# Optimization experiments

Measured on AMD Instinct MI355X. Metric: run time of the kernel, lower is better.

Reference implementation:

```python
import jax, jax.numpy as jnp
import numpy as np


def _filt2d(img, k):
    # 2D cross-correlation with OpenCV's default BORDER_REFLECT_101 padding.
    # img: [H, W], k: [3, 3]. XLA conv is cross-correlation (no flip), matching cv2.
    p = jnp.pad(img, 1, mode='reflect')  # reflect == REFLECT_101
    return jax.lax.conv_general_dilated(p[None, None], k[None, None],
                                        window_strides=(1, 1), padding='VALID')[0, 0]


def setup_inputs() -> dict:
    key = jax.random.key(0)
    k1, k2 = jax.random.split(key)
    pred = jax.random.normal(k1, (1, 1, 4096, 4096), dtype=jnp.float32)
    target = jax.random.normal(k2, (1, 1, 4096, 4096), dtype=jnp.float32)
    return {"pred": pred, "target": target}


def reference(pred, target):
    alpha = 0.2  # forward default
    # ---- masked MSE over target > 0 (named MAE in the original) ----
    valid = target > 0
    diff = jnp.where(valid, target - pred, 0.0)
    n_valid = jnp.maximum(jnp.sum(valid), 1)
    mae = jnp.sum(diff * diff) / n_valid.astype(diff.dtype)
    # ---- edge term: GaussianBlur(3x3, sigma=0) then Sobel x/y (cv2 semantics) ----
    g1 = jnp.array([0.25, 0.5, 0.25], jnp.float32)  # cv2 fixed 3-tap Gaussian
    blur_k = jnp.outer(g1, g1)
    smooth = jnp.array([1.0, 2.0, 1.0], jnp.float32)
    deriv = jnp.array([-1.0, 0.0, 1.0], jnp.float32)
    sob_x = jnp.outer(smooth, deriv)   # d/dx: smooth rows, differentiate cols
    sob_y = jnp.outer(deriv, smooth)   # d/dy
    p2 = jnp.squeeze(pred)   # [H, W]
    t2 = jnp.squeeze(target)
    pb = _filt2d(p2, blur_k)
    tb = _filt2d(t2, blur_k)
    dx = _filt2d(pb, sob_x) - _filt2d(tb, sob_x)
    dy = _filt2d(pb, sob_y) - _filt2d(tb, sob_y)
    # NOTE: original subtracts the y term (as written in the source) — kept faithfully.
    G = jnp.mean(dx * dx - dy * dy)
    # In torch the edge term goes through a numpy round-trip (no gradient).
    G = jax.lax.stop_gradient(G)
    return alpha * G + (1.0 - alpha) * mae
```

## Files before the change

kernel.cpp:

```cpp
#include <hip/hip_runtime.h>


#define TW 256
#define TH 32
#define LROWS 36
#define LW 264

__device__ __forceinline__ int reflect101(int i, int n) {
    if (i < 0) i = -i;
    if (i >= n) i = 2 * n - 2 - i;
    return i;
}

__device__ __forceinline__ void async16(const float* g, float* l) {
    __builtin_amdgcn_global_load_lds(
        (const __attribute__((address_space(1))) void*)g,
        (__attribute__((address_space(3))) void*)l,
        16, 0, 0);
}

__global__ __launch_bounds__(256) void loss_main(
    const float* __restrict__ pred, const float* __restrict__ target,
    double* __restrict__ part, int H, int W)
{
    __shared__ float psh[LROWS][LW];
    __shared__ float tsh[LROWS][LW];
    __shared__ float partials[4][3];

    const int tid  = threadIdx.x;
    const int lane = tid & 63;
    const int w    = tid >> 6;
    const int r0 = blockIdx.y * TH;
    const int c0 = blockIdx.x * TW;

#pragma unroll
    for (int j = 0; j < 18; ++j) {
        const int idx = j * 4 + w;
        const int row = (j >= 9) ? idx - 36 : idx;
        const int gr  = reflect101(r0 - 2 + row, H);
        const size_t goff = (size_t)gr * W + c0 + lane * 4;
        if (j >= 9) async16(target + goff, &tsh[row][4]);
        else        async16(pred   + goff, &psh[row][4]);
    }

    if (tid < 144) {
        const int row = tid >> 2;
        const int hc  = tid & 3;
        const int lc  = (hc < 2) ? (2 + hc) : (258 + hc);
        const int gc  = reflect101((hc < 2) ? (c0 - 2 + hc)
                                            : (c0 + 254 + hc), W);
        const int gr  = reflect101(r0 - 2 + row, H);
        const size_t off = (size_t)gr * W + gc;
        psh[row][lc] = pred[off];
        tsh[row][lc] = target[off];
    }
    __syncthreads();

    const int cg = lane;
    const int rb = w * 8;
    float mse = 0.f, cnt = 0.f, g = 0.f;

    float4 D0, D1, D2, D3, D4, S0, S1, S2, S3, S4;

    auto hpass = [&](int rw, bool doMse, float4& D_, float4& S_) {
        const float4 p0 = *(const float4*)&psh[rw][4 * cg];
        const float4 p1 = *(const float4*)&psh[rw][4 * cg + 4];
        const float4 p2 = *(const float4*)&psh[rw][4 * cg + 8];
        const float4 t0 = *(const float4*)&tsh[rw][4 * cg];
        const float4 t1 = *(const float4*)&tsh[rw][4 * cg + 4];
        const float4 t2 = *(const float4*)&tsh[rw][4 * cg + 8];
        const float e0z = p0.z - t0.z, e0w = p0.w - t0.w;
        const float e1x = p1.x - t1.x, e1y = p1.y - t1.y;
        const float e1z = p1.z - t1.z, e1w = p1.w - t1.w;
        const float e2x = p2.x - t2.x, e2y = p2.y - t2.y;
        D_.x = 0.25f * (e1z - e0z) + 0.5f * (e1y - e0w);
        D_.y = 0.25f * (e1w - e0w) + 0.5f * (e1z - e1x);
        D_.z = 0.25f * (e2x - e1x) + 0.5f * (e1w - e1y);
        D_.w = 0.25f * (e2y - e1y) + 0.5f * (e2x - e1z);
        S_.x = 0.25f * (e0z + e1z) + (e0w + e1y) + 1.5f * e1x;
        S_.y = 0.25f * (e0w + e1w) + (e1x + e1z) + 1.5f * e1y;
        S_.z = 0.25f * (e1x + e2x) + (e1y + e1w) + 1.5f * e1z;
        S_.w = 0.25f * (e1y + e2y) + (e1z + e2x) + 1.5f * e1w;
        if (doMse) {
            if (t1.x > 0.f) { mse += e1x * e1x; cnt += 1.f; }
            if (t1.y > 0.f) { mse += e1y * e1y; cnt += 1.f; }
            if (t1.z > 0.f) { mse += e1z * e1z; cnt += 1.f; }
            if (t1.w > 0.f) { mse += e1w * e1w; cnt += 1.f; }
        }
    };

    hpass(rb + 0, false, D0, S0);
    hpass(rb + 1, false, D1, S1);
    hpass(rb + 2, true,  D2, S2);
    hpass(rb + 3, true,  D3, S3);

#pragma unroll
    for (int k = 0; k < 8; ++k) {
        hpass(rb + 4 + k, (k < 6), D4, S4);
        const float dx0 = 0.25f * (D0.x + D4.x) + (D1.x + D3.x) + 1.5f * D2.x;
        const float dx1 = 0.25f * (D0.y + D4.y) + (D1.y + D3.y) + 1.5f * D2.y;
        const float dx2 = 0.25f * (D0.z + D4.z) + (D1.z + D3.z) + 1.5f * D2.z;
        const float dx3 = 0.25f * (D0.w + D4.w) + (D1.w + D3.w) + 1.5f * D2.w;
        const float dy0 = 0.25f * (S4.x - S0.x) + 0.5f * (S3.x - S1.x);
        const float dy1 = 0.25f * (S4.y - S0.y) + 0.5f * (S3.y - S1.y);
        const float dy2 = 0.25f * (S4.z - S0.z) + 0.5f * (S3.z - S1.z);
        const float dy3 = 0.25f * (S4.w - S0.w) + 0.5f * (S3.w - S1.w);
        g += (dx0 * dx0 - dy0 * dy0) + (dx1 * dx1 - dy1 * dy1)
           + (dx2 * dx2 - dy2 * dy2) + (dx3 * dx3 - dy3 * dy3);
        D0 = D1; D1 = D2; D2 = D3; D3 = D4;
        S0 = S1; S1 = S2; S2 = S3; S3 = S4;
    }

    for (int off = 32; off > 0; off >>= 1) {
        mse += __shfl_down(mse, off, 64);
        cnt += __shfl_down(cnt, off, 64);
        g   += __shfl_down(g,   off, 64);
    }
    if (lane == 0) {
        partials[w][0] = mse;
        partials[w][1] = cnt;
        partials[w][2] = g;
    }
    __syncthreads();
    if (tid == 0) {
        float m = 0.f, c2 = 0.f, gg = 0.f;
        for (int wv = 0; wv < 4; ++wv) {
            m  += partials[wv][0];
            c2 += partials[wv][1];
            gg += partials[wv][2];
        }
        const int bid = blockIdx.y * gridDim.x + blockIdx.x;
        double* slot = part + 3 * bid;
        slot[0] = (double)m;
        slot[1] = (double)c2;
        slot[2] = (double)gg;
    }
}

__global__ __launch_bounds__(256) void loss_final(
    const double* __restrict__ part, int nslots,
    float* __restrict__ out, double inv_hw)
{
    __shared__ double red[4][3];
    double m = 0.0, c = 0.0, g = 0.0;
    for (int s = threadIdx.x; s < nslots; s += 256) {
        m += part[3 * s];
        c += part[3 * s + 1];
        g += part[3 * s + 2];
    }
    for (int off = 32; off > 0; off >>= 1) {
        m += __shfl_down(m, off, 64);
        c += __shfl_down(c, off, 64);
        g += __shfl_down(g, off, 64);
    }
    const int w = threadIdx.x >> 6;
    if ((threadIdx.x & 63) == 0) { red[w][0] = m; red[w][1] = c; red[w][2] = g; }
    __syncthreads();
    if (threadIdx.x == 0) {
        m = red[0][0] + red[1][0] + red[2][0] + red[3][0];
        c = red[0][1] + red[1][1] + red[2][1] + red[3][1];
        g = red[0][2] + red[1][2] + red[2][2] + red[3][2];
        const double cnt = c < 1.0 ? 1.0 : c;
        out[0] = (float)(0.2 * (g * inv_hw) + 0.8 * (m / cnt));
    }
}

extern "C" void kernel_launch(void* const* d_in, const int* in_sizes, int n_in,
                              void* d_out, int out_size, void* d_ws, size_t ws_size,
                              hipStream_t stream) {
    const float* pred   = (const float*)d_in[0];
    const float* target = (const float*)d_in[1];
    float* out   = (float*)d_out;
    double* part = (double*)d_ws;

    const int H = 4096, W = 4096;
    const int nblocks = (W / TW) * (H / TH);

    dim3 grid(W / TW, H / TH);
    loss_main<<<grid, 256, 0, stream>>>(pred, target, part, H, W);
    loss_final<<<1, 256, 0, stream>>>(part, nblocks, out,
                                      1.0 / ((double)H * (double)W));
}
```

Baseline: 147.0 us.

## Stage pred-target difference in single LDS tile via register loads

Replaces the async global-to-LDS loads of separate pred and target tiles with register float4 loads. The difference pred-target is computed once and stored in a single shared tile, relying on linearity of the filters. The masked MSE is computed during the staging pass, halving LDS footprint and LDS reads in the stencil pass. It trades the async direct-to-LDS path for register staging, which raises register pressure (18 float4 held) but may improve occupancy through the smaller LDS use.

```diff
diff --git a/kernel.cpp b/kernel.cpp
--- a/kernel.cpp
+++ b/kernel.cpp
@@ -12,19 +12,11 @@
     return i;
 }
 
-__device__ __forceinline__ void async16(const float* g, float* l) {
-    __builtin_amdgcn_global_load_lds(
-        (const __attribute__((address_space(1))) void*)g,
-        (__attribute__((address_space(3))) void*)l,
-        16, 0, 0);
-}
-
 __global__ __launch_bounds__(256) void loss_main(
     const float* __restrict__ pred, const float* __restrict__ target,
     double* __restrict__ part, int H, int W)
 {
-    __shared__ float psh[LROWS][LW];
-    __shared__ float tsh[LROWS][LW];
+    __shared__ float esh[LROWS][LW];
     __shared__ float partials[4][3];
 
     const int tid  = threadIdx.x;
@@ -33,70 +25,79 @@
     const int r0 = blockIdx.y * TH;
     const int c0 = blockIdx.x * TW;
 
-#pragma unroll
-    for (int j = 0; j < 18; ++j) {
-        const int idx = j * 4 + w;
-        const int row = (j >= 9) ? idx - 36 : idx;
-        const int gr  = reflect101(r0 - 2 + row, H);
-        const size_t goff = (size_t)gr * W + c0 + lane * 4;
-        if (j >= 9) async16(target + goff, &tsh[row][4]);
-        else        async16(pred   + goff, &psh[row][4]);
+    float mse = 0.f, cnt = 0.f, g = 0.f;
+
+    float hp = 0.f, ht = 0.f;
+    int hrow = 0, hlc = 0;
+    const bool hasHalo = (tid < 144);
+    if (hasHalo) {
+        hrow = tid >> 2;
+        const int hc = tid & 3;
+        hlc = (hc < 2) ? (2 + hc) : (258 + hc);
+        const int gc = reflect101((hc < 2) ? (c0 - 2 + hc)
+                                           : (c0 + 254 + hc), W);
+        const int gr = reflect101(r0 - 2 + hrow, H);
+        const size_t off = (size_t)gr * W + gc;
+        hp = pred[off];
+        ht = target[off];
     }
 
-    if (tid < 144) {
-        const int row = tid >> 2;
-        const int hc  = tid & 3;
-        const int lc  = (hc < 2) ? (2 + hc) : (258 + hc);
-        const int gc  = reflect101((hc < 2) ? (c0 - 2 + hc)
-                                            : (c0 + 254 + hc), W);
+    float4 pv[9], tv[9];
+#pragma unroll
+    for (int j = 0; j < 9; ++j) {
+        const int row = j * 4 + w;
         const int gr  = reflect101(r0 - 2 + row, H);
-        const size_t off = (size_t)gr * W + gc;
-        psh[row][lc] = pred[off];
-        tsh[row][lc] = target[off];
+        const size_t off = (size_t)gr * W + c0 + lane * 4;
+        pv[j] = *(const float4*)(pred   + off);
+        tv[j] = *(const float4*)(target + off);
     }
+#pragma unroll
+    for (int j = 0; j < 9; ++j) {
+        const int row = j * 4 + w;
+        float4 e;
+        e.x = pv[j].x - tv[j].x;
+        e.y = pv[j].y - tv[j].y;
+        e.z = pv[j].z - tv[j].z;
+        e.w = pv[j].w - tv[j].w;
+        *(float4*)&esh[row][4 + 4 * lane] = e;
+        if (row >= 2 && row < 34) {
+            if (tv[j].x > 0.f) { mse += e.x * e.x; cnt += 1.f; }
+            if (tv[j].y > 0.f) { mse += e.y * e.y; cnt += 1.f; }
+            if (tv[j].z > 0.f) { mse += e.z * e.z; cnt += 1.f; }
+            if (tv[j].w > 0.f) { mse += e.w * e.w; cnt += 1.f; }
+        }
+    }
+    if (hasHalo) esh[hrow][hlc] = hp - ht;
+
     __syncthreads();
 
     const int cg = lane;
     const int rb = w * 8;
-    float mse = 0.f, cnt = 0.f, g = 0.f;
 
     float4 D0, D1, D2, D3, D4, S0, S1, S2, S3, S4;
 
-    auto hpass = [&](int rw, bool doMse, float4& D_, float4& S_) {
-        const float4 p0 = *(const float4*)&psh[rw][4 * cg];
-        const float4 p1 = *(const float4*)&psh[rw][4 * cg + 4];
-        const float4 p2 = *(const float4*)&psh[rw][4 * cg + 8];
-        const float4 t0 = *(const float4*)&tsh[rw][4 * cg];
-        const float4 t1 = *(const float4*)&tsh[rw][4 * cg + 4];
-        const float4 t2 = *(const float4*)&tsh[rw][4 * cg + 8];
-        const float e0z = p0.z - t0.z, e0w = p0.w - t0.w;
-        const float e1x = p1.x - t1.x, e1y = p1.y - t1.y;
-        const float e1z = p1.z - t1.z, e1w = p1.w - t1.w;
-        const float e2x = p2.x - t2.x, e2y = p2.y - t2.y;
-        D_.x = 0.25f * (e1z - e0z) + 0.5f * (e1y - e0w);
-        D_.y = 0.25f * (e1w - e0w) + 0.5f * (e1z - e1x);
-        D_.z = 0.25f * (e2x - e1x) + 0.5f * (e1w - e1y);
-        D_.w = 0.25f * (e2y - e1y) + 0.5f * (e2x - e1z);
-        S_.x = 0.25f * (e0z + e1z) + (e0w + e1y) + 1.5f * e1x;
-        S_.y = 0.25f * (e0w + e1w) + (e1x + e1z) + 1.5f * e1y;
-        S_.z = 0.25f * (e1x + e2x) + (e1y + e1w) + 1.5f * e1z;
-        S_.w = 0.25f * (e1y + e2y) + (e1z + e2x) + 1.5f * e1w;
-        if (doMse) {
-            if (t1.x > 0.f) { mse += e1x * e1x; cnt += 1.f; }
-            if (t1.y > 0.f) { mse += e1y * e1y; cnt += 1.f; }
-            if (t1.z > 0.f) { mse += e1z * e1z; cnt += 1.f; }
-            if (t1.w > 0.f) { mse += e1w * e1w; cnt += 1.f; }
-        }
+    auto hpass = [&](int rw, float4& D_, float4& S_) {
+        const float4 a = *(const float4*)&esh[rw][4 * cg];
+        const float4 b = *(const float4*)&esh[rw][4 * cg + 4];
+        const float4 c = *(const float4*)&esh[rw][4 * cg + 8];
+        D_.x = 0.25f * (b.z - a.z) + 0.5f * (b.y - a.w);
+        D_.y = 0.25f * (b.w - a.w) + 0.5f * (b.z - b.x);
+        D_.z = 0.25f * (c.x - b.x) + 0.5f * (b.w - b.y);
+        D_.w = 0.25f * (c.y - b.y) + 0.5f * (c.x - b.z);
+        S_.x = 0.25f * (a.z + b.z) + (a.w + b.y) + 1.5f * b.x;
+        S_.y = 0.25f * (a.w + b.w) + (b.x + b.z) + 1.5f * b.y;
+        S_.z = 0.25f * (b.x + c.x) + (b.y + b.w) + 1.5f * b.z;
+        S_.w = 0.25f * (b.y + c.y) + (b.z + c.x) + 1.5f * b.w;
     };
 
-    hpass(rb + 0, false, D0, S0);
-    hpass(rb + 1, false, D1, S1);
-    hpass(rb + 2, true,  D2, S2);
-    hpass(rb + 3, true,  D3, S3);
+    hpass(rb + 0, D0, S0);
+    hpass(rb + 1, D1, S1);
+    hpass(rb + 2, D2, S2);
+    hpass(rb + 3, D3, S3);
 
 #pragma unroll
     for (int k = 0; k < 8; ++k) {
-        hpass(rb + 4 + k, (k < 6), D4, S4);
+        hpass(rb + 4 + k, D4, S4);
         const float dx0 = 0.25f * (D0.x + D4.x) + (D1.x + D3.x) + 1.5f * D2.x;
         const float dx1 = 0.25f * (D0.y + D4.y) + (D1.y + D3.y) + 1.5f * D2.y;
         const float dx2 = 0.25f * (D0.z + D4.z) + (D1.z + D3.z) + 1.5f * D2.z;
```

After: 150.0 us. 1.02x slower.

## Make blocks persistent over tile columns with double-buffered async LDS loads

Applied to the files above, without the earlier changes.

Each block now has 512 threads and walks 8 vertically stacked 256x32 tiles. It double-buffers the pred/target LDS tiles, issuing async global-to-LDS loads for tile i+2 while tile i is computed, and uses explicit vmcnt/lgkmcnt waits and s_barrier. This is meant to hide global load latency behind compute and to reduce per-block launch and halo overhead. The costs are far fewer blocks (256), one block per CU because of the doubled LDS, and fragile hand-written wait counts.

```diff
diff --git a/kernel.cpp b/kernel.cpp
--- a/kernel.cpp
+++ b/kernel.cpp
@@ -5,6 +5,7 @@
 #define TH 32
 #define LROWS 36
 #define LW 264
+#define NT 8
 
 __device__ __forceinline__ int reflect101(int i, int n) {
     if (i < 0) i = -i;
@@ -15,100 +16,137 @@
 __device__ __forceinline__ void async16(const float* g, float* l) {
     __builtin_amdgcn_global_load_lds(
         (const __attribute__((address_space(1))) void*)g,
-        (__attribute__((address_space(3))) void*)l,
-        16, 0, 0);
-}
-
-__global__ __launch_bounds__(256) void loss_main(
+        (__attribute__((address_space(3))) void*)l, 16, 0, 0);
+}
+
+#define SFENCE()  __builtin_amdgcn_sched_barrier(0)
+#define BAR()     asm volatile("s_barrier" ::: "memory")
+#define VMCNT10() asm volatile("s_waitcnt vmcnt(10)" ::: "memory")
+#define VMCNT0()  asm volatile("s_waitcnt vmcnt(0)" ::: "memory")
+#define LGKM0()   asm volatile("s_waitcnt lgkmcnt(0)" ::: "memory")
+
+__global__ __launch_bounds__(512, 1) void loss_main(
     const float* __restrict__ pred, const float* __restrict__ target,
     double* __restrict__ part, int H, int W)
 {
-    __shared__ float psh[LROWS][LW];
-    __shared__ float tsh[LROWS][LW];
-    __shared__ float partials[4][3];
+    __shared__ float bufP[2][LROWS][LW];
+    __shared__ float bufT[2][LROWS][LW];
+    __shared__ float partials[8][3];
 
     const int tid  = threadIdx.x;
     const int lane = tid & 63;
     const int w    = tid >> 6;
-    const int r0 = blockIdx.y * TH;
-    const int c0 = blockIdx.x * TW;
-
+    const int c0   = blockIdx.x * TW;
+    const int ty0  = blockIdx.y * NT;
+
+    int hvld = tid; if (hvld >= 288) hvld -= 288;
+    const int htsel = (hvld >= 144);
+    const int hrr   = hvld - (htsel ? 144 : 0);
+    const int hrow  = hrr >> 2;
+    const int hc    = hrr & 3;
+    const int hlc   = (hc < 2) ? (2 + hc) : (258 + hc);
+    const int hgc   = reflect101((hc < 2) ? (c0 - 2 + hc) : (c0 + 254 + hc), W);
+    const float* hsrc = htsel ? target : pred;
+
+    float mse = 0.f, cnt = 0.f, g = 0.f;
+
+    auto stage = [&](int ty, int bi) -> float {
+        const int r0 = ty * TH;
+        const float hv = *(volatile const float*)(hsrc +
+                         (size_t)reflect101(r0 - 2 + hrow, H) * W + hgc);
+        SFENCE();
 #pragma unroll
-    for (int j = 0; j < 18; ++j) {
-        const int idx = j * 4 + w;
-        const int row = (j >= 9) ? idx - 36 : idx;
-        const int gr  = reflect101(r0 - 2 + row, H);
-        const size_t goff = (size_t)gr * W + c0 + lane * 4;
-        if (j >= 9) async16(target + goff, &tsh[row][4]);
-        else        async16(pred   + goff, &psh[row][4]);
-    }
-
-    if (tid < 144) {
-        const int row = tid >> 2;
-        const int hc  = tid & 3;
-        const int lc  = (hc < 2) ? (2 + hc) : (258 + hc);
-        const int gc  = reflect101((hc < 2) ? (c0 - 2 + hc)
-                                            : (c0 + 254 + hc), W);
-        const int gr  = reflect101(r0 - 2 + row, H);
-        const size_t off = (size_t)gr * W + gc;
-        psh[row][lc] = pred[off];
-        tsh[row][lc] = target[off];
-    }
-    __syncthreads();
-
-    const int cg = lane;
-    const int rb = w * 8;
-    float mse = 0.f, cnt = 0.f, g = 0.f;
-
-    float4 D0, D1, D2, D3, D4, S0, S1, S2, S3, S4;
-
-    auto hpass = [&](int rw, bool doMse, float4& D_, float4& S_) {
-        const float4 p0 = *(const float4*)&psh[rw][4 * cg];
-        const float4 p1 = *(const float4*)&psh[rw][4 * cg + 4];
-        const float4 p2 = *(const float4*)&psh[rw][4 * cg + 8];
-        const float4 t0 = *(const float4*)&tsh[rw][4 * cg];
-        const float4 t1 = *(const float4*)&tsh[rw][4 * cg + 4];
-        const float4 t2 = *(const float4*)&tsh[rw][4 * cg + 8];
-        const float e0z = p0.z - t0.z, e0w = p0.w - t0.w;
-        const float e1x = p1.x - t1.x, e1y = p1.y - t1.y;
-        const float e1z = p1.z - t1.z, e1w = p1.w - t1.w;
-        const float e2x = p2.x - t2.x, e2y = p2.y - t2.y;
-        D_.x = 0.25f * (e1z - e0z) + 0.5f * (e1y - e0w);
-        D_.y = 0.25f * (e1w - e0w) + 0.5f * (e1z - e1x);
-        D_.z = 0.25f * (e2x - e1x) + 0.5f * (e1w - e1y);
-        D_.w = 0.25f * (e2y - e1y) + 0.5f * (e2x - e1z);
-        S_.x = 0.25f * (e0z + e1z) + (e0w + e1y) + 1.5f * e1x;
-        S_.y = 0.25f * (e0w + e1w) + (e1x + e1z) + 1.5f * e1y;
-        S_.z = 0.25f * (e1x + e2x) + (e1y + e1w) + 1.5f * e1z;
-        S_.w = 0.25f * (e1y + e2y) + (e1z + e2x) + 1.5f * e1w;
-        if (doMse) {
-            if (t1.x > 0.f) { mse += e1x * e1x; cnt += 1.f; }
-            if (t1.y > 0.f) { mse += e1y * e1y; cnt += 1.f; }
-            if (t1.z > 0.f) { mse += e1z * e1z; cnt += 1.f; }
-            if (t1.w > 0.f) { mse += e1w * e1w; cnt += 1.f; }
-        }
+        for (int j = 0; j < 9; ++j) {
+            const int idx = j * 8 + w;
+            const int row = (idx < 36) ? idx : idx - 36;
+            const int gr  = reflect101(r0 - 2 + row, H);
+            const size_t goff = (size_t)gr * W + c0 + lane * 4;
+            if (idx < 36) async16(pred   + goff, &bufP[bi][row][4]);
+            else          async16(target + goff, &bufT[bi][row][4]);
+        }
+        SFENCE();
+        return hv;
     };
 
-    hpass(rb + 0, false, D0, S0);
-    hpass(rb + 1, false, D1, S1);
-    hpass(rb + 2, true,  D2, S2);
-    hpass(rb + 3, true,  D3, S3);
+    auto write_halo = [&](int bi, float hv) {
+        float* base = htsel ? &bufT[bi][0][0] : &bufP[bi][0][0];
+        base[hrow * LW + hlc] = hv;
+    };
+
+    auto compute = [&](int bi) {
+        const int cg = lane;
+        const int rb = w * 4;
+        float4 D0, D1, D2, D3, D4, S0, S1, S2, S3, S4;
+
+        auto hpass = [&](int rw, bool doMse, float4& D_, float4& S_) {
+            const float4 p0 = *(const float4*)&bufP[bi][rw][4 * cg];
+            const float4 p1 = *(const float4*)&bufP[bi][rw][4 * cg + 4];
+            const float4 p2 = *(const float4*)&bufP[bi][rw][4 * cg + 8];
+            const float4 t0 = *(const float4*)&bufT[bi][rw][4 * cg];
+            const float4 t1 = *(const float4*)&bufT[bi][rw][4 * cg + 4];
+            const float4 t2 = *(const float4*)&bufT[bi][rw][4 * cg + 8];
+            const float e0z = p0.z - t0.z, e0w = p0.w - t0.w;
+            const float e1x = p1.x - t1.x, e1y = p1.y - t1.y;
+            const float e1z = p1.z - t1.z, e1w = p1.w - t1.w;
+            const float e2x = p2.x - t2.x, e2y = p2.y - t2.y;
+            D_.x = 0.25f * (e1z - e0z) + 0.5f * (e1y - e0w);
+            D_.y = 0.25f * (e1w - e0w) + 0.5f * (e1z - e1x);
+            D_.z = 0.25f * (e2x - e1x) + 0.5f * (e1w - e1y);
+            D_.w = 0.25f * (e2y - e1y) + 0.5f * (e2x - e1z);
+            S_.x = 0.25f * (e0z + e1z) + (e0w + e1y) + 1.5f * e1x;
+            S_.y = 0.25f * (e0w + e1w) + (e1x + e1z) + 1.5f * e1y;
+            S_.z = 0.25f * (e1x + e2x) + (e1y + e1w) + 1.5f * e1z;
+            S_.w = 0.25f * (e1y + e2y) + (e1z + e2x) + 1.5f * e1w;
+            if (doMse) {
+                if (t1.x > 0.f) { mse += e1x * e1x; cnt += 1.f; }
+                if (t1.y > 0.f) { mse += e1y * e1y; cnt += 1.f; }
+                if (t1.z > 0.f) { mse += e1z * e1z; cnt += 1.f; }
+                if (t1.w > 0.f) { mse += e1w * e1w; cnt += 1.f; }
+            }
+        };
+
+        hpass(rb + 0, false, D0, S0);
+        hpass(rb + 1, false, D1, S1);
+        hpass(rb + 2, true,  D2, S2);
+        hpass(rb + 3, true,  D3, S3);
 
 #pragma unroll
-    for (int k = 0; k < 8; ++k) {
-        hpass(rb + 4 + k, (k < 6), D4, S4);
-        const float dx0 = 0.25f * (D0.x + D4.x) + (D1.x + D3.x) + 1.5f * D2.x;
-        const float dx1 = 0.25f * (D0.y + D4.y) + (D1.y + D3.y) + 1.5f * D2.y;
-        const float dx2 = 0.25f * (D0.z + D4.z) + (D1.z + D3.z) + 1.5f * D2.z;
-        const float dx3 = 0.25f * (D0.w + D4.w) + (D1.w + D3.w) + 1.5f * D2.w;
-        const float dy0 = 0.25f * (S4.x - S0.x) + 0.5f * (S3.x - S1.x);
-        const float dy1 = 0.25f * (S4.y - S0.y) + 0.5f * (S3.y - S1.y);
-        const float dy2 = 0.25f * (S4.z - S0.z) + 0.5f * (S3.z - S1.z);
-        const float dy3 = 0.25f * (S4.w - S0.w) + 0.5f * (S3.w - S1.w);
-        g += (dx0 * dx0 - dy0 * dy0) + (dx1 * dx1 - dy1 * dy1)
-           + (dx2 * dx2 - dy2 * dy2) + (dx3 * dx3 - dy3 * dy3);
-        D0 = D1; D1 = D2; D2 = D3; D3 = D4;
-        S0 = S1; S1 = S2; S2 = S3; S3 = S4;
+        for (int k = 0; k < 4; ++k) {
+            hpass(rb + 4 + k, (k < 2), D4, S4);
+            const float dx0 = 0.25f * (D0.x + D4.x) + (D1.x + D3.x) + 1.5f * D2.x;
+            const float dx1 = 0.25f * (D0.y + D4.y) + (D1.y + D3.y) + 1.5f * D2.y;
+            const float dx2 = 0.25f * (D0.z + D4.z) + (D1.z + D3.z) + 1.5f * D2.z;
+            const float dx3 = 0.25f * (D0.w + D4.w) + (D1.w + D3.w) + 1.5f * D2.w;
+            const float dy0 = 0.25f * (S4.x - S0.x) + 0.5f * (S3.x - S1.x);
+            const float dy1 = 0.25f * (S4.y - S0.y) + 0.5f * (S3.y - S1.y);
+            const float dy2 = 0.25f * (S4.z - S0.z) + 0.5f * (S3.z - S1.z);
+            const float dy3 = 0.25f * (S4.w - S0.w) + 0.5f * (S3.w - S1.w);
+            g += (dx0 * dx0 - dy0 * dy0) + (dx1 * dx1 - dy1 * dy1)
+               + (dx2 * dx2 - dy2 * dy2) + (dx3 * dx3 - dy3 * dy3);
+            D0 = D1; D1 = D2; D2 = D3; D3 = D4;
+            S0 = S1; S1 = S2; S2 = S3; S3 = S4;
+        }
+    };
+
+    float hv0 = stage(ty0 + 0, 0);
+    float hv1 = stage(ty0 + 1, 1);
+    write_halo(0, hv0);
+    VMCNT10(); LGKM0(); BAR(); SFENCE();
+
+#pragma unroll
+    for (int i = 0; i < NT; ++i) {
+        const int cur = i & 1;
+        if (i + 1 < NT)
+            write_halo(cur ^ 1, (cur ^ 1) ? hv1 : hv0);
+        compute(cur);
+        if (i + 2 < NT) {
+            BAR(); SFENCE();
+            if (cur) hv1 = stage(ty0 + i + 2, cur);
+            else     hv0 = stage(ty0 + i + 2, cur);
+            VMCNT10(); LGKM0(); BAR(); SFENCE();
+        } else if (i + 1 < NT) {
+            VMCNT0(); LGKM0(); BAR(); SFENCE();
+        }
     }
 
     for (int off = 32; off > 0; off >>= 1) {
@@ -124,7 +162,7 @@
     __syncthreads();
     if (tid == 0) {
         float m = 0.f, c2 = 0.f, gg = 0.f;
-        for (int wv = 0; wv < 4; ++wv) {
+        for (int wv = 0; wv < 8; ++wv) {
             m  += partials[wv][0];
             c2 += partials[wv][1];
             gg += partials[wv][2];
@@ -174,10 +212,10 @@
     double* part = (double*)d_ws;
 
     const int H = 4096, W = 4096;
-    const int nblocks = (W / TW) * (H / TH);
-
-    dim3 grid(W / TW, H / TH);
-    loss_main<<<grid, 256, 0, stream>>>(pred, target, part, H, W);
+    dim3 grid(W / TW, H / (TH * NT));
+    const int nblocks = grid.x * grid.y;
+
+    loss_main<<<grid, 512, 0, stream>>>(pred, target, part, H, W);
     loss_final<<<1, 256, 0, stream>>>(part, nblocks, out,
                                       1.0 / ((double)H * (double)W));
 }
```

New measurement: 161.1 us. 9.6% more time.
